# Optimization experiments

Hardware: AMD Instinct MI355X
Metric: run time of the kernel (lower is better)

Reference implementation:

```python
import jax, jax.numpy as jnp
import numpy as np

B, N, F = 4096, 128, 3
EPS = 1e-5


def _bn(x, g, b):
    # BatchNorm1d(element_num) on [B, N, C]: channels are dim 1 (the N elements);
    # training-mode stats over dims (0, 2), biased variance (torch default).
    m = x.mean(axis=(0, 2), keepdims=True)
    v = ((x - m) ** 2).mean(axis=(0, 2), keepdims=True)
    return (x - m) / jnp.sqrt(v + EPS) * g[None, :, None] + b[None, :, None]


def _rel(x, W, bvec, psi, phi, wr):
    # f'_i = wr/N * sum_{j != i} (psi*phi * <x_i, x_j>) * relu(unary(x_j))
    n = x.shape[1]
    U = jax.nn.relu(jnp.einsum('bnd,ed->bne', x, W) + bvec)       # [B,N,D]
    S = (psi * phi) * jnp.einsum('bnd,bmd->bnm', x, x)            # [B,N,N]
    S = S * (1.0 - jnp.eye(n, dtype=x.dtype))                     # exclude j == i
    return wr * jnp.einsum('bnm,bmd->bnd', S, U) / n


def setup_inputs() -> dict:
    key = jax.random.key(0)
    ks = iter(jax.random.split(key, 64))
    d1, d2 = 2 * F, 4 * F  # 6, 12

    def w(shape, s=0.1):
        return (jax.random.normal(next(ks), shape, dtype=jnp.float32) * s)

    def scalar():
        return jax.random.uniform(next(ks), (), dtype=jnp.float32)

    inp = {
        'x': jax.random.normal(next(ks), (B, N, F), dtype=jnp.float32),
        'fc1_w': w((d1, F)), 'fc1_b': w((d1,)),
        'bn1_g': jnp.ones((N,), jnp.float32), 'bn1_b': jnp.zeros((N,), jnp.float32),
        'fc2_w': w((d2, d1)), 'fc2_b': w((d2,)),
        'bn2_g': jnp.ones((N,), jnp.float32), 'bn2_b': jnp.zeros((N,), jnp.float32),
        'fc3_w': w((d2, d2)), 'fc3_b': w((d2,)),
        'u1_w': w((d2, d2)), 'u1_b': w((d2,)), 'ps1': scalar(), 'ph1': scalar(), 'wr1': scalar(),
        'u2_w': w((d2, d2)), 'u2_b': w((d2,)), 'ps2': scalar(), 'ph2': scalar(), 'wr2': scalar(),
        'u3_w': w((d2, d2)), 'u3_b': w((d2,)), 'ps3': scalar(), 'ph3': scalar(), 'wr3': scalar(),
        'u4_w': w((d2, d2)), 'u4_b': w((d2,)), 'ps4': scalar(), 'ph4': scalar(), 'wr4': scalar(),
        'fc4_w': w((d1, d2)), 'fc4_b': w((d1,)),
        'bn4_g': jnp.ones((N,), jnp.float32), 'bn4_b': jnp.zeros((N,), jnp.float32),
        'fc5_w': w((F, d1)), 'fc5_b': w((F,)),
        'fc6_w': w((1, F)), 'fc6_b': w((1,)),
        'fc7_w': w((F - 1, F)), 'fc7_b': w((F - 1,)),
        'fc8_w': w((1, F)), 'fc8_b': w((1,)),
    }
    return inp


def reference(x, fc1_w, fc1_b, bn1_g, bn1_b, fc2_w, fc2_b, bn2_g, bn2_b,
              fc3_w, fc3_b,
              u1_w, u1_b, ps1, ph1, wr1,
              u2_w, u2_b, ps2, ph2, wr2,
              u3_w, u3_b, ps3, ph3, wr3,
              u4_w, u4_b, ps4, ph4, wr4,
              fc4_w, fc4_b, bn4_g, bn4_b,
              fc5_w, fc5_b, fc6_w, fc6_b, fc7_w, fc7_b, fc8_w, fc8_b):
    h = jax.nn.relu(_bn(jnp.einsum('bnf,ef->bne', x, fc1_w) + fc1_b, bn1_g, bn1_b))
    h = jax.nn.relu(_bn(jnp.einsum('bnf,ef->bne', h, fc2_w) + fc2_b, bn2_g, bn2_b))
    h = jax.nn.sigmoid(jnp.einsum('bnf,ef->bne', h, fc3_w) + fc3_b)
    h = _rel(h, u1_w, u1_b, ps1, ph1, wr1)
    h = _rel(h, u2_w, u2_b, ps2, ph2, wr2)
    h = _rel(h, u3_w, u3_b, ps3, ph3, wr3)
    h = _rel(h, u4_w, u4_b, ps4, ph4, wr4)
    h = jax.nn.relu(_bn(jnp.einsum('bnf,ef->bne', h, fc4_w) + fc4_b, bn4_g, bn4_b))
    h = jax.nn.relu(jnp.einsum('bnf,ef->bne', h, fc5_w) + fc5_b)
    cls = jnp.einsum('bnf,ef->bne', h, fc6_w) + fc6_b          # [B,N,1]
    geo = jnp.einsum('bnf,ef->bne', h, fc7_w) + fc7_b          # [B,N,F-1]
    res = jnp.concatenate([cls, geo], axis=2)                   # [B,N,F]
    pres = res.max(axis=1)                                      # MaxPool1d over all N -> [B,F]
    pred = jax.nn.sigmoid(pres @ fc8_w.T + fc8_b)               # [B,1]
    return pred
```

## Files before the change

kernel.cpp:

```cpp
#include <hip/hip_runtime.h>
#include <hip/hip_fp16.h>

#define BB 4096
#define NN 128
#define EPS 1e-5f

#define S1 0
#define S2 2048
#define S4 4096
#define ST_FLOATS 6144
#define A4_OFF 6144

static __device__ __forceinline__ float sigmoidf_(float z){
  return 1.f/(1.f+__expf(-z));
}

__global__ __launch_bounds__(256) void k1(const float* __restrict__ x, const float* __restrict__ w1,
                   const float* __restrict__ b1, float* __restrict__ st){
  __shared__ float bl[512];
  const int t = threadIdx.x;
  const int tid = blockIdx.x*256 + t;
  float W[18], Bv[6];
  #pragma unroll
  for (int i=0;i<18;i++) W[i]=w1[i];
  #pragma unroll
  for (int i=0;i<6;i++) Bv[i]=b1[i];
  float s=0.f, sq=0.f;
  #pragma unroll
  for (int kk=0;kk<2;kk++){
    const int r = tid + kk*262144;
    const float* xr = x + (size_t)r*3;
    float x0=xr[0], x1=xr[1], x2=xr[2];
    #pragma unroll
    for (int e=0;e<6;e++){
      float a = fmaf(x0,W[e*3+0], fmaf(x1,W[e*3+1], fmaf(x2,W[e*3+2], Bv[e])));
      s+=a; sq=fmaf(a,a,sq);
    }
  }
  bl[t]=s; bl[256+t]=sq;
  __syncthreads();
  const int shadow = (blockIdx.x & 7)*256;
  if (t<128) atomicAdd(&st[S1+shadow+t], bl[t]+bl[t+128]);
  else       atomicAdd(&st[S1+shadow+t], bl[t+128]+bl[t+256]);
}

__global__ __launch_bounds__(256) void k2(const float* __restrict__ x,
                   const float* __restrict__ w1, const float* __restrict__ b1,
                   const float* __restrict__ g1, const float* __restrict__ bb1,
                   const float* __restrict__ w2, const float* __restrict__ b2,
                   float* __restrict__ st){
  __shared__ float bl[512];
  const int t = threadIdx.x;
  const int tid = blockIdx.x*256 + t;
  const int n = t & 127;
  float ss=0.f, qs=0.f;
  #pragma unroll
  for (int c=0;c<8;c++){ ss+=st[S1+c*256+n]; qs+=st[S1+c*256+128+n]; }
  const float mean = ss*(1.f/(BB*6));
  const float var  = qs*(1.f/(BB*6)) - mean*mean;
  const float sc = g1[n]*rsqrtf(var+EPS), sh = bb1[n]-mean*sc;
  float W1[18], B1v[6], W2[72], B2v[12];
  #pragma unroll
  for (int i=0;i<18;i++) W1[i]=w1[i];
  #pragma unroll
  for (int i=0;i<6;i++) B1v[i]=b1[i];
  #pragma unroll
  for (int i=0;i<72;i++) W2[i]=w2[i];
  #pragma unroll
  for (int i=0;i<12;i++) B2v[i]=b2[i];
  float s=0.f, sq=0.f;
  #pragma unroll
  for (int kk=0;kk<2;kk++){
    const int r = tid + kk*262144;
    const float* xr = x + (size_t)r*3;
    float x0=xr[0], x1=xr[1], x2=xr[2];
    float h[6];
    #pragma unroll
    for (int e=0;e<6;e++){
      float a = fmaf(x0,W1[e*3+0], fmaf(x1,W1[e*3+1], fmaf(x2,W1[e*3+2], B1v[e])));
      h[e]=fmaxf(fmaf(a,sc,sh),0.f);
    }
    #pragma unroll
    for (int d=0;d<12;d++){
      float z=B2v[d];
      #pragma unroll
      for (int e=0;e<6;e++) z=fmaf(h[e],W2[d*6+e],z);
      s+=z; sq=fmaf(z,z,sq);
    }
  }
  bl[t]=s; bl[256+t]=sq;
  __syncthreads();
  const int shadow = (blockIdx.x & 7)*256;
  if (t<128) atomicAdd(&st[S2+shadow+t], bl[t]+bl[t+128]);
  else       atomicAdd(&st[S2+shadow+t], bl[t+128]+bl[t+256]);
}

__global__ __launch_bounds__(256) void k3(
  const float* __restrict__ x,
  const float* __restrict__ w1, const float* __restrict__ b1,
  const float* __restrict__ g1, const float* __restrict__ bb1,
  const float* __restrict__ w2, const float* __restrict__ b2,
  const float* __restrict__ g2, const float* __restrict__ bb2,
  const float* __restrict__ w3, const float* __restrict__ b3,
  const float* __restrict__ u1w, const float* __restrict__ u1b,
  const float* __restrict__ ps1, const float* __restrict__ ph1, const float* __restrict__ wr1,
  const float* __restrict__ u2w, const float* __restrict__ u2b,
  const float* __restrict__ ps2, const float* __restrict__ ph2, const float* __restrict__ wr2,
  const float* __restrict__ u3w, const float* __restrict__ u3b,
  const float* __restrict__ ps3, const float* __restrict__ ph3, const float* __restrict__ wr3,
  const float* __restrict__ u4w, const float* __restrict__ u4b,
  const float* __restrict__ ps4, const float* __restrict__ ph4, const float* __restrict__ wr4,
  const float* __restrict__ w4, const float* __restrict__ b4,
  float* __restrict__ a4, float* __restrict__ st)
{
  __shared__ float lds[4][2304];
  const int wave = threadIdx.x >> 6;
  const int lane = threadIdx.x & 63;
  const int b = blockIdx.x*4 + wave;
  float* Us = &lds[wave][0];
  __half* Xs = (__half*)&lds[wave][1536];
  const int r0 = lane*2, r1 = r0+1;

  float s1a=0,q1a=0,s1b=0,q1b=0,s2a=0,q2a=0,s2b=0,q2b=0;
  #pragma unroll
  for (int c=0;c<8;c++){
    s1a+=st[S1+c*256+r0]; q1a+=st[S1+c*256+128+r0];
    s1b+=st[S1+c*256+r1]; q1b+=st[S1+c*256+128+r1];
    s2a+=st[S2+c*256+r0]; q2a+=st[S2+c*256+128+r0];
    s2b+=st[S2+c*256+r1]; q2b+=st[S2+c*256+128+r1];
  }
  const float inv1 = 1.f/(BB*6), inv2 = 1.f/(BB*12);
  float m = s1a*inv1, v = q1a*inv1 - m*m;
  const float sA0 = g1[r0]*rsqrtf(v+EPS), hA0 = bb1[r0]-m*sA0;
  m = s1b*inv1; v = q1b*inv1 - m*m;
  const float sA1 = g1[r1]*rsqrtf(v+EPS), hA1 = bb1[r1]-m*sA1;
  m = s2a*inv2; v = q2a*inv2 - m*m;
  const float sB0 = g2[r0]*rsqrtf(v+EPS), hB0 = bb2[r0]-m*sB0;
  m = s2b*inv2; v = q2b*inv2 - m*m;
  const float sB1 = g2[r1]*rsqrtf(v+EPS), hB1 = bb2[r1]-m*sB1;

  const float2* xr = (const float2*)(x + ((size_t)b*128 + r0)*3);
  float2 c0=xr[0], c1=xr[1], c2=xr[2];
  const float xa0=c0.x, xa1=c0.y, xa2=c1.x;
  const float xb0=c1.y, xb1=c2.x, xb2=c2.y;

  float X0[12], X1[12];
  {
    float g6a[6], g6b[6];
    #pragma unroll
    for (int e=0;e<6;e++){
      float a0 = fmaf(xa0,w1[e*3+0], fmaf(xa1,w1[e*3+1], fmaf(xa2,w1[e*3+2], b1[e])));
      float a1v= fmaf(xb0,w1[e*3+0], fmaf(xb1,w1[e*3+1], fmaf(xb2,w1[e*3+2], b1[e])));
      g6a[e]=fmaxf(fmaf(a0,sA0,hA0),0.f);
      g6b[e]=fmaxf(fmaf(a1v,sA1,hA1),0.f);
    }
    float h0[12], h1[12];
    #pragma unroll
    for (int d=0;d<12;d++){
      float z0=b2[d], z1=b2[d];
      #pragma unroll
      for (int e=0;e<6;e++){ z0=fmaf(g6a[e],w2[d*6+e],z0); z1=fmaf(g6b[e],w2[d*6+e],z1); }
      h0[d]=fmaxf(fmaf(z0,sB0,hB0),0.f);
      h1[d]=fmaxf(fmaf(z1,sB1,hB1),0.f);
    }
    #pragma unroll
    for (int d=0; d<12; d++){
      float z0=b3[d], z1=b3[d];
      #pragma unroll
      for (int e=0;e<12;e++){ z0=fmaf(h0[e],w3[d*12+e],z0); z1=fmaf(h1[e],w3[d*12+e],z1); }
      X0[d]=sigmoidf_(z0); X1[d]=sigmoidf_(z1);
    }
  }

  const float* UW[4]  = {u1w,u2w,u3w,u4w};
  const float* UBv[4] = {u1b,u2b,u3b,u4b};
  const float cf[4] = {
    wr1[0]*ps1[0]*ph1[0]*(1.f/128.f),
    wr2[0]*ps2[0]*ph2[0]*(1.f/128.f),
    wr3[0]*ps3[0]*ph3[0]*(1.f/128.f),
    wr4[0]*ps4[0]*ph4[0]*(1.f/128.f)
  };

  const int g = lane>>4;
  int kc = lane & 15; if (kc>11) kc=11;

  #pragma unroll
  for (int l=0;l<4;l++){
    const float* uw = UW[l];
    const float* ub = UBv[l];
    float Y0[12], Y1[12];
    {
      float U0[12], U1[12];
      #pragma unroll
      for (int d=0;d<12;d++){
        float z0=ub[d], z1=ub[d];
        #pragma unroll
        for (int e=0;e<12;e++){ z0=fmaf(X0[e],uw[d*12+e],z0); z1=fmaf(X1[e],uw[d*12+e],z1); }
        U0[d]=fmaxf(z0,0.f); U1[d]=fmaxf(z1,0.f);
      }
      float q0=0.f, q1=0.f;
      #pragma unroll
      for (int e=0;e<12;e++){ q0=fmaf(X0[e],X0[e],q0); q1=fmaf(X1[e],X1[e],q1); }
      float4* uwr = (float4*)(Us + r0*12);
      uwr[0]=make_float4(U0[0],U0[1],U0[2],U0[3]);
      uwr[1]=make_float4(U0[4],U0[5],U0[6],U0[7]);
      uwr[2]=make_float4(U0[8],U0[9],U0[10],U0[11]);
      uwr[3]=make_float4(U1[0],U1[1],U1[2],U1[3]);
      uwr[4]=make_float4(U1[4],U1[5],U1[6],U1[7]);
      uwr[5]=make_float4(U1[8],U1[9],U1[10],U1[11]);
      __half2 hp[12];
      #pragma unroll
      for (int i=0;i<6;i++) hp[i]   = __floats2half2_rn(X0[2*i],X0[2*i+1]);
      #pragma unroll
      for (int i=0;i<6;i++) hp[6+i] = __floats2half2_rn(X1[2*i],X1[2*i+1]);
      {
        const uint4* hpv = (const uint4*)hp;
        uint4* xw = (uint4*)(Xs + r0*12);
        xw[0]=hpv[0]; xw[1]=hpv[1]; xw[2]=hpv[2];
      }
      #pragma unroll
      for (int d=0;d<12;d++){ Y0[d] = -q0*U0[d]; Y1[d] = -q1*U1[d]; }
    }

    float mp[12];
    #pragma unroll
    for (int d=0;d<12;d++) mp[d]=0.f;
    #pragma unroll
    for (int i=0;i<32;i++){
      const int n = (g<<5) + ((i+g)&31);
      const float xv = __half2float(Xs[n*12 + kc]);
      const float4* up = (const float4*)(Us + n*12);
      float4 u0=up[0], u1=up[1], u2=up[2];
      mp[0]=fmaf(xv,u0.x,mp[0]); mp[1]=fmaf(xv,u0.y,mp[1]); mp[2]=fmaf(xv,u0.z,mp[2]); mp[3]=fmaf(xv,u0.w,mp[3]);
      mp[4]=fmaf(xv,u1.x,mp[4]); mp[5]=fmaf(xv,u1.y,mp[5]); mp[6]=fmaf(xv,u1.z,mp[6]); mp[7]=fmaf(xv,u1.w,mp[7]);
      mp[8]=fmaf(xv,u2.x,mp[8]); mp[9]=fmaf(xv,u2.y,mp[9]); mp[10]=fmaf(xv,u2.z,mp[10]); mp[11]=fmaf(xv,u2.w,mp[11]);
    }
    #pragma unroll
    for (int d=0;d<12;d++) mp[d] += __shfl_xor(mp[d], 16, 64);
    #pragma unroll
    for (int d=0;d<12;d++) mp[d] += __shfl_xor(mp[d], 32, 64);

    #pragma unroll
    for (int k=0;k<12;k++){
      const float xa = X0[k], xb = X1[k];
      #pragma unroll
      for (int d=0;d<12;d++){
        const float mv = __int_as_float(__builtin_amdgcn_readlane(__float_as_int(mp[d]), k));
        Y0[d]=fmaf(xa,mv,Y0[d]); Y1[d]=fmaf(xb,mv,Y1[d]);
      }
    }
    const float coef = cf[l];
    #pragma unroll
    for (int d=0;d<12;d++){ X0[d]=coef*Y0[d]; X1[d]=coef*Y1[d]; }
  }

  float z0[6], z1[6];
  float s0=0.f,sq0=0.f,s1=0.f,sq1=0.f;
  #pragma unroll
  for (int e=0;e<6;e++){
    float a0=b4[e], a1v=b4[e];
    #pragma unroll
    for (int d=0;d<12;d++){ a0=fmaf(X0[d],w4[e*12+d],a0); a1v=fmaf(X1[d],w4[e*12+d],a1v); }
    z0[e]=a0; z1[e]=a1v;
    s0+=a0; sq0=fmaf(a0,a0,sq0); s1+=a1v; sq1=fmaf(a1v,a1v,sq1);
  }
  float4* aw = (float4*)(a4 + ((size_t)b*128 + r0)*6);
  aw[0]=make_float4(z0[0],z0[1],z0[2],z0[3]);
  aw[1]=make_float4(z0[4],z0[5],z1[0],z1[1]);
  aw[2]=make_float4(z1[2],z1[3],z1[4],z1[5]);

  __syncthreads();
  lds[wave][r0]=s0; lds[wave][r1]=s1;
  lds[wave][128+r0]=sq0; lds[wave][128+r1]=sq1;
  __syncthreads();
  const int t = threadIdx.x;
  const int c = (blockIdx.x & 7)*256;
  atomicAdd(&st[S4 + c + t], lds[0][t]+lds[1][t]+lds[2][t]+lds[3][t]);
}

__global__ __launch_bounds__(256) void k4(
  const float* __restrict__ a4, const float* __restrict__ g4, const float* __restrict__ bb4,
  const float* __restrict__ w5, const float* __restrict__ b5,
  const float* __restrict__ w6, const float* __restrict__ b6,
  const float* __restrict__ w7, const float* __restrict__ b7,
  const float* __restrict__ w8, const float* __restrict__ b8,
  const float* __restrict__ st, float* __restrict__ out)
{
  const int wave = threadIdx.x>>6, lane = threadIdx.x&63;
  const int b = blockIdx.x*4 + wave;
  const int r0 = lane*2, r1 = r0+1;
  float ss0=0.f, qq0=0.f, ss1=0.f, qq1=0.f;
  #pragma unroll
  for (int cc=0;cc<8;cc++){
    ss0 += st[S4+cc*256+r0];     qq0 += st[S4+cc*256+128+r0];
    ss1 += st[S4+cc*256+r1];     qq1 += st[S4+cc*256+128+r1];
  }
  const float inv = 1.f/(BB*6);
  const float mean0 = ss0*inv, var0 = qq0*inv - mean0*mean0;
  const float sc0 = g4[r0]*rsqrtf(var0+EPS), sh0 = bb4[r0]-mean0*sc0;
  const float mean1 = ss1*inv, var1 = qq1*inv - mean1*mean1;
  const float sc1 = g4[r1]*rsqrtf(var1+EPS), sh1 = bb4[r1]-mean1*sc1;

  const float4* ar = (const float4*)(a4 + ((size_t)b*128 + r0)*6);
  float4 p0=ar[0], p1=ar[1], p2=ar[2];
  float h0[6] = {p0.x,p0.y,p0.z,p0.w,p1.x,p1.y};
  float h1[6] = {p1.z,p1.w,p2.x,p2.y,p2.z,p2.w};
  #pragma unroll
  for (int e=0;e<6;e++){
    h0[e]=fmaxf(fmaf(h0[e],sc0,sh0),0.f);
    h1[e]=fmaxf(fmaf(h1[e],sc1,sh1),0.f);
  }
  float mx[3];
  {
    float h5a[3], h5b[3];
    #pragma unroll
    for (int f=0;f<3;f++){
      float za=b5[f], zb=b5[f];
      #pragma unroll
      for (int e=0;e<6;e++){ za=fmaf(h0[e],w5[f*6+e],za); zb=fmaf(h1[e],w5[f*6+e],zb); }
      h5a[f]=fmaxf(za,0.f); h5b[f]=fmaxf(zb,0.f);
    }
    float ca=b6[0], cb=b6[0];
    float g0a=b7[0], g0b=b7[0], g1a=b7[1], g1b=b7[1];
    #pragma unroll
    for (int f=0;f<3;f++){
      ca=fmaf(h5a[f],w6[f],ca);   cb=fmaf(h5b[f],w6[f],cb);
      g0a=fmaf(h5a[f],w7[f],g0a); g0b=fmaf(h5b[f],w7[f],g0b);
      g1a=fmaf(h5a[f],w7[3+f],g1a); g1b=fmaf(h5b[f],w7[3+f],g1b);
    }
    mx[0]=fmaxf(ca,cb); mx[1]=fmaxf(g0a,g0b); mx[2]=fmaxf(g1a,g1b);
  }
  #pragma unroll
  for (int off=32; off>0; off>>=1){
    mx[0]=fmaxf(mx[0], __shfl_xor(mx[0],off,64));
    mx[1]=fmaxf(mx[1], __shfl_xor(mx[1],off,64));
    mx[2]=fmaxf(mx[2], __shfl_xor(mx[2],off,64));
  }
  if (lane==0){
    float z = b8[0] + mx[0]*w8[0] + mx[1]*w8[1] + mx[2]*w8[2];
    out[b]=sigmoidf_(z);
  }
}

extern "C" void kernel_launch(void* const* d_in, const int* in_sizes, int n_in,
                              void* d_out, int out_size, void* d_ws, size_t ws_size,
                              hipStream_t stream){
  const float* x   = (const float*)d_in[0];
  const float* f1w = (const float*)d_in[1];
  const float* f1b = (const float*)d_in[2];
  const float* g1  = (const float*)d_in[3];
  const float* bb1 = (const float*)d_in[4];
  const float* f2w = (const float*)d_in[5];
  const float* f2b = (const float*)d_in[6];
  const float* g2  = (const float*)d_in[7];
  const float* bb2 = (const float*)d_in[8];
  const float* f3w = (const float*)d_in[9];
  const float* f3b = (const float*)d_in[10];
  const float* u1w = (const float*)d_in[11];
  const float* u1b = (const float*)d_in[12];
  const float* ps1 = (const float*)d_in[13];
  const float* ph1 = (const float*)d_in[14];
  const float* wr1 = (const float*)d_in[15];
  const float* u2w = (const float*)d_in[16];
  const float* u2b = (const float*)d_in[17];
  const float* ps2 = (const float*)d_in[18];
  const float* ph2 = (const float*)d_in[19];
  const float* wr2 = (const float*)d_in[20];
  const float* u3w = (const float*)d_in[21];
  const float* u3b = (const float*)d_in[22];
  const float* ps3 = (const float*)d_in[23];
  const float* ph3 = (const float*)d_in[24];
  const float* wr3 = (const float*)d_in[25];
  const float* u4w = (const float*)d_in[26];
  const float* u4b = (const float*)d_in[27];
  const float* ps4 = (const float*)d_in[28];
  const float* ph4 = (const float*)d_in[29];
  const float* wr4 = (const float*)d_in[30];
  const float* f4w = (const float*)d_in[31];
  const float* f4b = (const float*)d_in[32];
  const float* g4  = (const float*)d_in[33];
  const float* bb4 = (const float*)d_in[34];
  const float* f5w = (const float*)d_in[35];
  const float* f5b = (const float*)d_in[36];
  const float* f6w = (const float*)d_in[37];
  const float* f6b = (const float*)d_in[38];
  const float* f7w = (const float*)d_in[39];
  const float* f7b = (const float*)d_in[40];
  const float* f8w = (const float*)d_in[41];
  const float* f8b = (const float*)d_in[42];

  float* wsf = (float*)d_ws;
  float* st  = wsf;
  float* a4  = wsf + A4_OFF;
  float* out = (float*)d_out;

  hipMemsetAsync(st, 0, ST_FLOATS*sizeof(float), stream);
  k1<<<dim3(1024), dim3(256), 0, stream>>>(x, f1w, f1b, st);
  k2<<<dim3(1024), dim3(256), 0, stream>>>(x, f1w, f1b, g1, bb1, f2w, f2b, st);
  k3<<<dim3(1024), dim3(256), 0, stream>>>(x, f1w, f1b, g1, bb1, f2w, f2b, g2, bb2,
      f3w, f3b,
      u1w,u1b,ps1,ph1,wr1, u2w,u2b,ps2,ph2,wr2,
      u3w,u3b,ps3,ph3,wr3, u4w,u4b,ps4,ph4,wr4,
      f4w, f4b, a4, st);
  k4<<<dim3(1024), dim3(256), 0, stream>>>(a4, g4, bb4, f5w, f5b,
      f6w, f6b, f7w, f7b, f8w, f8b, st, out);
}
```

Before: 223.4 us.

## Pack relation-layer X and U as paired fp16 and use fdot2 accumulation

Stores the per-row unary outputs U in LDS as fp16 instead of fp32, and packs rows in pairs (row 2k, 2k+1) so each 32-bit word holds the same feature for two rows. The X^T·U accumulation loop then takes 16 iterations of v_dot2 (fp16 pairs, fp32 accumulate) instead of 32 fp32 FMA iterations, which halves LDS traffic and instruction count and shrinks the shared buffer. In exchange U loses precision through fp16 rounding, which could hurt accuracy.

```diff
diff --git a/kernel.cpp b/kernel.cpp
--- a/kernel.cpp
+++ b/kernel.cpp
@@ -13,6 +13,27 @@
 
 static __device__ __forceinline__ float sigmoidf_(float z){
   return 1.f/(1.f+__expf(-z));
+}
+
+static __device__ __forceinline__ float fdot2_(unsigned a, unsigned b, float c){
+#if defined(__has_builtin)
+#if __has_builtin(__builtin_amdgcn_fdot2)
+  typedef _Float16 h2v __attribute__((ext_vector_type(2)));
+  h2v av = *reinterpret_cast<h2v*>(&a);
+  h2v bv = *reinterpret_cast<h2v*>(&b);
+  return __builtin_amdgcn_fdot2(av, bv, c, false);
+#else
+  __half2 ah = *reinterpret_cast<__half2*>(&a);
+  __half2 bh = *reinterpret_cast<__half2*>(&b);
+  float2 af = __half22float2(ah), bf = __half22float2(bh);
+  return fmaf(af.y, bf.y, fmaf(af.x, bf.x, c));
+#endif
+#else
+  __half2 ah = *reinterpret_cast<__half2*>(&a);
+  __half2 bh = *reinterpret_cast<__half2*>(&b);
+  float2 af = __half22float2(ah), bf = __half22float2(bh);
+  return fmaf(af.y, bf.y, fmaf(af.x, bf.x, c));
+#endif
 }
 
 __global__ __launch_bounds__(256) void k1(const float* __restrict__ x, const float* __restrict__ w1,
@@ -113,12 +134,12 @@
   const float* __restrict__ w4, const float* __restrict__ b4,
   float* __restrict__ a4, float* __restrict__ st)
 {
-  __shared__ float lds[4][2304];
+  __shared__ float lds[4][1536];
   const int wave = threadIdx.x >> 6;
   const int lane = threadIdx.x & 63;
   const int b = blockIdx.x*4 + wave;
-  float* Us = &lds[wave][0];
-  __half* Xs = (__half*)&lds[wave][1536];
+  unsigned* Xp = (unsigned*)&lds[wave][0];
+  unsigned* Up = (unsigned*)&lds[wave][768];
   const int r0 = lane*2, r1 = r0+1;
 
   float s1a=0,q1a=0,s1b=0,q1b=0,s2a=0,q2a=0,s2b=0,q2b=0;
@@ -201,22 +222,19 @@
       float q0=0.f, q1=0.f;
       #pragma unroll
       for (int e=0;e<12;e++){ q0=fmaf(X0[e],X0[e],q0); q1=fmaf(X1[e],X1[e],q1); }
-      float4* uwr = (float4*)(Us + r0*12);
-      uwr[0]=make_float4(U0[0],U0[1],U0[2],U0[3]);
-      uwr[1]=make_float4(U0[4],U0[5],U0[6],U0[7]);
-      uwr[2]=make_float4(U0[8],U0[9],U0[10],U0[11]);
-      uwr[3]=make_float4(U1[0],U1[1],U1[2],U1[3]);
-      uwr[4]=make_float4(U1[4],U1[5],U1[6],U1[7]);
-      uwr[5]=make_float4(U1[8],U1[9],U1[10],U1[11]);
-      __half2 hp[12];
-      #pragma unroll
-      for (int i=0;i<6;i++) hp[i]   = __floats2half2_rn(X0[2*i],X0[2*i+1]);
-      #pragma unroll
-      for (int i=0;i<6;i++) hp[6+i] = __floats2half2_rn(X1[2*i],X1[2*i+1]);
+      __half2 hp[12], up[12];
+      #pragma unroll
+      for (int e=0;e<12;e++){
+        hp[e] = __floats2half2_rn(X0[e],X1[e]);
+        up[e] = __floats2half2_rn(U0[e],U1[e]);
+      }
       {
         const uint4* hpv = (const uint4*)hp;
-        uint4* xw = (uint4*)(Xs + r0*12);
+        const uint4* upv = (const uint4*)up;
+        uint4* xw = (uint4*)(Xp + lane*12);
+        uint4* uwp = (uint4*)(Up + lane*12);
         xw[0]=hpv[0]; xw[1]=hpv[1]; xw[2]=hpv[2];
+        uwp[0]=upv[0]; uwp[1]=upv[1]; uwp[2]=upv[2];
       }
       #pragma unroll
       for (int d=0;d<12;d++){ Y0[d] = -q0*U0[d]; Y1[d] = -q1*U1[d]; }
@@ -226,14 +244,17 @@
     #pragma unroll
     for (int d=0;d<12;d++) mp[d]=0.f;
     #pragma unroll
-    for (int i=0;i<32;i++){
-      const int n = (g<<5) + ((i+g)&31);
-      const float xv = __half2float(Xs[n*12 + kc]);
-      const float4* up = (const float4*)(Us + n*12);
-      float4 u0=up[0], u1=up[1], u2=up[2];
-      mp[0]=fmaf(xv,u0.x,mp[0]); mp[1]=fmaf(xv,u0.y,mp[1]); mp[2]=fmaf(xv,u0.z,mp[2]); mp[3]=fmaf(xv,u0.w,mp[3]);
-      mp[4]=fmaf(xv,u1.x,mp[4]); mp[5]=fmaf(xv,u1.y,mp[5]); mp[6]=fmaf(xv,u1.z,mp[6]); mp[7]=fmaf(xv,u1.w,mp[7]);
-      mp[8]=fmaf(xv,u2.x,mp[8]); mp[9]=fmaf(xv,u2.y,mp[9]); mp[10]=fmaf(xv,u2.z,mp[10]); mp[11]=fmaf(xv,u2.w,mp[11]);
+    for (int i=0;i<16;i++){
+      const int p = (g<<4) | ((i+g)&15);
+      const unsigned xv2 = Xp[p*12 + kc];
+      const uint4* urow = (const uint4*)(Up + p*12);
+      uint4 ua=urow[0], ub4=urow[1], uc=urow[2];
+      mp[0]=fdot2_(xv2, ua.x, mp[0]);  mp[1]=fdot2_(xv2, ua.y, mp[1]);
+      mp[2]=fdot2_(xv2, ua.z, mp[2]);  mp[3]=fdot2_(xv2, ua.w, mp[3]);
+      mp[4]=fdot2_(xv2, ub4.x, mp[4]); mp[5]=fdot2_(xv2, ub4.y, mp[5]);
+      mp[6]=fdot2_(xv2, ub4.z, mp[6]); mp[7]=fdot2_(xv2, ub4.w, mp[7]);
+      mp[8]=fdot2_(xv2, uc.x, mp[8]);  mp[9]=fdot2_(xv2, uc.y, mp[9]);
+      mp[10]=fdot2_(xv2, uc.z, mp[10]); mp[11]=fdot2_(xv2, uc.w, mp[11]);
     }
     #pragma unroll
     for (int d=0;d<12;d++) mp[d] += __shfl_xor(mp[d], 16, 64);
```

Measured after the change: 209.0 us. -6.4%, faster.
